# Kernel tuning notes

Measured on AMD Instinct MI355X. Metric: run time of the kernel, lower is better.

The kernel has to match this reference:

```python
import jax, jax.numpy as jnp
import numpy as np

L_DEG = 4      # max out-degree L
DEPTH = 7      # complete L-ary tree depth -> 21845 nodes
N_GEN = 16
C_ST = 8
M_LAB = 256


def _build_tree():
    sizes = [L_DEG ** d for d in range(DEPTH + 1)]
    limits = np.concatenate([[0], np.cumsum(sizes)]).astype(np.int64)
    t_size = int(limits[-1])
    nodes = np.arange(t_size)
    rng = np.random.default_rng(0)
    labels = rng.integers(0, M_LAB, t_size)
    parent = np.where(nodes > 0, (nodes - 1) // L_DEG, 0)
    pos = np.where(nodes > 0, (nodes - 1) % L_DEG, 0)
    ch = np.zeros((t_size, L_DEG), dtype=np.int64)
    n_internal = int(limits[-2])
    ch[:n_internal] = L_DEG * nodes[:n_internal, None] + np.arange(1, L_DEG + 1)[None, :]
    t = np.concatenate([labels[:, None], parent[:, None], pos[:, None], ch], axis=1).astype(np.int64)
    return t, limits


def setup_inputs() -> dict:
    key = jax.random.key(0)
    ka, kb, kp, ks = jax.random.split(key, 4)
    t, limits = _build_tree()
    return {
        "t": jnp.asarray(t),
        "t_limits": jnp.asarray(limits),
        "a": jax.random.normal(ka, (N_GEN, C_ST, C_ST, L_DEG), dtype=jnp.float32),
        "b": jax.random.normal(kb, (N_GEN, C_ST, M_LAB), dtype=jnp.float32),
        "pi": jax.random.normal(kp, (N_GEN, C_ST, L_DEG), dtype=jnp.float32),
        "sp": jax.random.normal(ks, (N_GEN, L_DEG), dtype=jnp.float32),
    }


def _forward(tn, lim, a, b, pi, sp):
    # tn, lim are host numpy int arrays (tree structure is a constant).
    G, C, _, L = a.shape
    t_size = int(lim[-1])
    n_levels = len(lim) - 1
    sL = int(lim[-2])                      # first leaf index
    labels = tn[:, 0]
    posf = tn[:, 2]
    ch_all = tn[:, 3:3 + L]

    sm_a = jax.nn.softmax(a, axis=1)       # P(parent_state i | child_state j, pos l)
    sm_b = jax.nn.softmax(b, axis=2)
    sm_pi = jax.nn.softmax(pi, axis=1)
    sm_sp = jax.nn.softmax(sp, axis=1)
    a_sp = sm_a * sm_sp[:, None, None, :]  # [G,i,j,L]

    # ---------------- upward pass ----------------
    prior = jnp.zeros((t_size, G, C), a.dtype)
    beta = jnp.zeros((t_size, G, C), a.dtype)
    beta_il = jnp.zeros((t_size, G, C), a.dtype)

    prior_lv = jnp.moveaxis(sm_pi[:, :, posf[sL:]], 2, 0)   # [NL,G,C]
    emis_lv = jnp.moveaxis(sm_b[:, :, labels[sL:]], 2, 0)   # [NL,G,C]
    beta_lv = prior_lv * emis_lv
    beta_lv = beta_lv / jnp.sum(beta_lv, axis=2, keepdims=True)
    prior = prior.at[sL:].set(prior_lv)
    beta = beta.at[sL:].set(beta_lv)

    for lev in range(n_levels - 2, -1, -1):   # internal levels, bottom-up
        s, e = int(lim[lev]), int(lim[lev + 1])
        ch = ch_all[s:e]                       # [P,L]
        mask = (ch > 0).astype(a.dtype)        # children packed in first slots
        prior_ch = prior[ch]                   # [P,L,G,C]
        beta_ch = beta[ch]                     # [P,L,G,C]
        u_prior = jnp.einsum('gijl,pl,plgj->pgi', a_sp, mask, prior_ch)
        u_bil = jnp.einsum('gijl,pl,plgj->pgi', a_sp, mask, beta_ch) / u_prior
        emis = jnp.moveaxis(sm_b[:, :, labels[s:e]], 2, 0)  # [P,G,C]
        tmp = emis * u_bil * u_prior
        u_beta = tmp / jnp.sum(tmp, axis=2, keepdims=True)
        prior = prior.at[s:e].set(u_prior)
        beta = beta.at[s:e].set(u_beta)
        beta_il = beta_il.at[s:e].set(u_bil)

    # ---------------- downward pass ----------------
    # row t_size is a dummy slot for padded (absent) children
    eps_i = jnp.zeros((t_size + 1, G, C), a.dtype).at[0].set(beta[0])
    eps_ijl = jnp.zeros((t_size, G, C, C, L), a.dtype)
    for lev in range(0, n_levels - 1):         # parents, top-down (root included)
        s, e = int(lim[lev]), int(lim[lev + 1])
        ch = ch_all[s:e]
        maskb = ch > 0
        mask = maskb.astype(a.dtype)
        beta_ch = jnp.transpose(beta[ch], (0, 2, 3, 1))       # [P,G,Cj,L]
        pe = eps_i[s:e] / (prior[s:e] * beta_il[s:e])         # [P,G,Ci]
        res = (pe[:, :, :, None, None] * a_sp[None]
               * beta_ch[:, :, None, :, :]
               * mask[:, None, None, None, :])                # [P,G,i,j,L]
        child_eps = jnp.sum(res, axis=3)                       # sum over j (as in source) -> [P,G,i,L]
        vals = jnp.moveaxis(child_eps, 3, 1).reshape(-1, G, C) # [P*L,G,C]
        safe = np.where(maskb, ch, t_size).reshape(-1)
        eps_i = eps_i.at[safe].set(vals)
        eps_ijl = eps_ijl.at[s:e].set(res)
    eps_i = eps_i[:t_size]
    # leaves' eps_ijl stay zero (source scatters zeros there)

    # ---------------- log-likelihood ----------------
    a_lh = jnp.einsum('ugijl,gijl->g', eps_ijl, jnp.log(sm_a))
    b_lh = jnp.einsum('ugc,gcu->g', eps_i, jnp.log(sm_b)[:, :, labels])
    pi_lh = jnp.einsum('ugc,gcu->g', eps_i[sL:], jnp.log(sm_pi)[:, :, posf[sL:]])
    eps_l = jnp.sum(eps_ijl, axis=(2, 3))                      # [u,g,L]
    sp_lh = jnp.einsum('ugl,gl->g', eps_l, jnp.log(sm_sp))
    return a_lh + b_lh + pi_lh + sp_lh


def reference(t, t_limits, a, b, pi, sp):
    tn = np.asarray(t)
    lim = np.asarray(t_limits)
    return _forward(tn, lim, a, b, pi, sp)
```

## Files before the change

### kernel.cpp

```cpp
#include <hip/hip_runtime.h>


#define G 16
#define C 8
#define GC 128
#define TSIZE 21845
#define SL 5461

__device__ __forceinline__ float grp8_sum(float v) {
  v += __shfl_xor(v, 1);
  v += __shfl_xor(v, 2);
  v += __shfl_xor(v, 4);
  return v;
}

__global__ void setup_kernel(const float* __restrict__ ain, const float* __restrict__ bin,
                             const float* __restrict__ piin, const float* __restrict__ spin,
                             float* __restrict__ a_sp, float* __restrict__ log_a,
                             float* __restrict__ sm_bT, float* __restrict__ log_bT,
                             float* __restrict__ sm_piT, float* __restrict__ log_piT,
                             float* __restrict__ log_sp, float* __restrict__ out) {
  int blk = blockIdx.x, tid = threadIdx.x;
  if (blk < 16) {
    int g = blk;
    __shared__ float red4[4];
    for (int c = 0; c < 8; ++c) {
      int row = g * 8 + c;
      float x = bin[row * 256 + tid];
      float m = x;
      #pragma unroll
      for (int off2 = 32; off2; off2 >>= 1) m = fmaxf(m, __shfl_xor(m, off2));
      if ((tid & 63) == 0) red4[tid >> 6] = m;
      __syncthreads();
      m = fmaxf(fmaxf(red4[0], red4[1]), fmaxf(red4[2], red4[3]));
      __syncthreads();
      float e = expf(x - m);
      float ssum = e;
      #pragma unroll
      for (int off2 = 32; off2; off2 >>= 1) ssum += __shfl_xor(ssum, off2);
      if ((tid & 63) == 0) red4[tid >> 6] = ssum;
      __syncthreads();
      ssum = red4[0] + red4[1] + red4[2] + red4[3];
      __syncthreads();
      sm_bT[tid * GC + row]  = e / ssum;
      log_bT[tid * GC + row] = (x - m) - logf(ssum);
    }
  } else if (blk == 16) {
    for (int col = tid; col < 512; col += 256) {
      int g = col >> 5, j = (col >> 2) & 7, l = col & 3;
      float x[8], m = -1e30f;
      #pragma unroll
      for (int i = 0; i < 8; ++i) { x[i] = ain[g*256 + i*32 + j*4 + l]; m = fmaxf(m, x[i]); }
      float ssum = 0.f;
      #pragma unroll
      for (int i = 0; i < 8; ++i) ssum += expf(x[i] - m);
      float ls = logf(ssum);
      float y0 = spin[g*4+0], y1 = spin[g*4+1], y2 = spin[g*4+2], y3 = spin[g*4+3];
      float ms = fmaxf(fmaxf(y0, y1), fmaxf(y2, y3));
      float d = expf(y0-ms) + expf(y1-ms) + expf(y2-ms) + expf(y3-ms);
      float spv = expf(spin[g*4+l] - ms) / d;
      #pragma unroll
      for (int i = 0; i < 8; ++i) {
        int o2 = g*256 + i*32 + j*4 + l;
        float smv = expf(x[i] - m) / ssum;
        a_sp[o2]  = smv * spv;
        log_a[o2] = (x[i] - m) - ls;
      }
    }
  } else {
    if (tid < 64) {
      int g = tid >> 2, l = tid & 3;
      float x[8], m = -1e30f;
      #pragma unroll
      for (int c = 0; c < 8; ++c) { x[c] = piin[g*32 + c*4 + l]; m = fmaxf(m, x[c]); }
      float ssum = 0.f;
      #pragma unroll
      for (int c = 0; c < 8; ++c) ssum += expf(x[c] - m);
      float ls = logf(ssum);
      #pragma unroll
      for (int c = 0; c < 8; ++c) {
        sm_piT[l*GC + g*8 + c]  = expf(x[c] - m) / ssum;
        log_piT[l*GC + g*8 + c] = (x[c] - m) - ls;
      }
    } else if (tid < 80) {
      int g = tid - 64;
      float y[4], m = -1e30f;
      #pragma unroll
      for (int l = 0; l < 4; ++l) { y[l] = spin[g*4 + l]; m = fmaxf(m, y[l]); }
      float ssum = 0.f;
      #pragma unroll
      for (int l = 0; l < 4; ++l) ssum += expf(y[l] - m);
      float ls = logf(ssum);
      #pragma unroll
      for (int l = 0; l < 4; ++l) log_sp[g*4 + l] = (y[l] - m) - ls;
    } else if (tid < 96) {
      out[tid - 80] = 0.0f;
    }
  }
}

__device__ __forceinline__ void up_lds(int v, int lab, int gi, int g8,
    const float* asp, const float* __restrict__ sm_bT,
    float* sBeta, float* sNum, bool wantNum) {
  int ch0 = 4*v + 1;
  float ub = 0.f;
  #pragma unroll
  for (int l = 0; l < 4; ++l) {
    const float4* bp = (const float4*)(sBeta + (ch0 + l)*GC + g8);
    float4 b0 = bp[0], b1 = bp[1];
    ub += asp[l]*b0.x + asp[4+l]*b0.y + asp[8+l]*b0.z + asp[12+l]*b0.w
        + asp[16+l]*b1.x + asp[20+l]*b1.y + asp[24+l]*b1.z + asp[28+l]*b1.w;
  }
  float tmp = sm_bT[lab*GC + gi] * ub;
  float s = grp8_sum(tmp);
  sBeta[v*GC + gi] = tmp / s;
  if (wantNum) sNum[v*GC + gi] = ub;
}

__device__ __forceinline__ double down_lds(int v, int lab, float e, int gi, int g8,
    const float* asp, const float* aal, const float* lsp,
    const float* __restrict__ log_bT, float* sBeta, const float* sNum) {
  float pe = e / sNum[v*GC + gi];
  int ch0 = 4*v + 1;
  float local = 0.f;
  #pragma unroll
  for (int l = 0; l < 4; ++l) {
    float4* bp = (float4*)(sBeta + (ch0 + l)*GC + g8);
    float4 b0 = bp[0], b1 = bp[1];
    float S = asp[l]*b0.x + asp[4+l]*b0.y + asp[8+l]*b0.z + asp[12+l]*b0.w
            + asp[16+l]*b1.x + asp[20+l]*b1.y + asp[24+l]*b1.z + asp[28+l]*b1.w;
    float A = aal[l]*b0.x + aal[4+l]*b0.y + aal[8+l]*b0.z + aal[12+l]*b0.w
            + aal[16+l]*b1.x + aal[20+l]*b1.y + aal[24+l]*b1.z + aal[28+l]*b1.w;
    float ce = pe * S;
    sBeta[(ch0 + l)*GC + gi] = ce;
    local += pe*A + ce*lsp[l];
  }
  return (double)local + (double)(e * log_bT[lab*GC + gi]);
}

__global__ __launch_bounds__(512, 1) void up_kernel(
    const float* __restrict__ a_sp, const float* __restrict__ sm_bT,
    const float* __restrict__ sm_piT, const int* __restrict__ t,
    float* __restrict__ betaG) {
  __shared__ float sBeta[85*GC];
  const int blk = blockIdx.x, tid = threadIdx.x;
  const int gi = tid & 127, g = gi >> 3, i = gi & 7, g8 = g*8, w = tid >> 7;
  float asp[32];
  {
    const float4* pa = (const float4*)(a_sp + g*256 + i*32);
    #pragma unroll
    for (int q = 0; q < 8; ++q) {
      float4 v = pa[q];
      asp[q*4+0]=v.x; asp[q*4+1]=v.y; asp[q*4+2]=v.z; asp[q*4+3]=v.w;
    }
  }
  const int base_leaf = SL + blk*64;
  #pragma unroll
  for (int it = 0; it < 16; ++it) {
    int k = it*4 + w;
    float bt = sm_piT[(k & 3)*GC + gi] * sm_bT[t[(base_leaf + k)*7]*GC + gi];
    float s = grp8_sum(bt);
    sBeta[(21 + k)*GC + gi] = bt / s;
  }
  __syncthreads();
  #pragma unroll
  for (int it = 0; it < 4; ++it) {
    int k = it*4 + w;
    up_lds(5 + k, t[(1365 + blk*16 + k)*7], gi, g8, asp, sm_bT, sBeta, nullptr, false);
  }
  __syncthreads();
  up_lds(1 + w, t[(341 + blk*4 + w)*7], gi, g8, asp, sm_bT, sBeta, nullptr, false);
  __syncthreads();
  if (tid < 128) {
    up_lds(0, t[(85 + blk)*7], gi, g8, asp, sm_bT, sBeta, nullptr, false);
    betaG[(size_t)(85 + blk)*GC + gi] = sBeta[gi];
  }
}

__global__ __launch_bounds__(512, 1) void downall_kernel(
    const float* __restrict__ a_sp, const float* __restrict__ log_a,
    const float* __restrict__ log_sp, const float* __restrict__ sm_bT,
    const float* __restrict__ log_bT, const float* __restrict__ sm_piT,
    const float* __restrict__ log_piT, const int* __restrict__ t,
    const float* __restrict__ betaG, float* __restrict__ out) {
  __shared__ float  sBeta[85*GC];
  __shared__ float  sNum[21*GC];
  __shared__ float  sEps[GC];
  __shared__ double sd[64];
  const int blk = blockIdx.x, tid = threadIdx.x;
  const int gi = tid & 127, g = gi >> 3, i = gi & 7, g8 = g*8, w = tid >> 7;
  float asp[32], aal[32], lsp[4];
  {
    const float4* pa = (const float4*)(a_sp  + g*256 + i*32);
    const float4* pl = (const float4*)(log_a + g*256 + i*32);
    #pragma unroll
    for (int k = 0; k < 8; ++k) {
      float4 va = pa[k], vl = pl[k];
      asp[k*4+0]=va.x; asp[k*4+1]=va.y; asp[k*4+2]=va.z; asp[k*4+3]=va.w;
      aal[k*4+0]=va.x*vl.x; aal[k*4+1]=va.y*vl.y; aal[k*4+2]=va.z*vl.z; aal[k*4+3]=va.w*vl.w;
    }
    #pragma unroll
    for (int l = 0; l < 4; ++l) lsp[l] = log_sp[g*4 + l];
  }

  #pragma unroll
  for (int it = 0; it < 16; ++it) {
    int k = it*4 + w, u = 21 + k;
    int ch0 = 4*u + 1;
    float ub = 0.f;
    #pragma unroll
    for (int l = 0; l < 4; ++l) {
      const float4* bp = (const float4*)(betaG + (size_t)(ch0 + l)*GC + g8);
      float4 b0 = bp[0], b1 = bp[1];
      ub += asp[l]*b0.x + asp[4+l]*b0.y + asp[8+l]*b0.z + asp[12+l]*b0.w
          + asp[16+l]*b1.x + asp[20+l]*b1.y + asp[24+l]*b1.z + asp[28+l]*b1.w;
    }
    float tmp = sm_bT[t[u*7]*GC + gi] * ub;
    float s = grp8_sum(tmp);
    sBeta[u*GC + gi] = tmp / s;
  }
  __syncthreads();
  #pragma unroll
  for (int it = 0; it < 4; ++it) {
    int u = 5 + it*4 + w;
    up_lds(u, t[u*7], gi, g8, asp, sm_bT, sBeta, sNum, true);
  }
  __syncthreads();
  up_lds(1 + w, t[(1 + w)*7], gi, g8, asp, sm_bT, sBeta, sNum, true);
  __syncthreads();
  if (tid < 128)
    up_lds(0, t[0], gi, g8, asp, sm_bT, sBeta, sNum, true);
  __syncthreads();

  if (tid < 128) {
    int a1 = 1 + (blk >> 6), a2 = 5 + (blk >> 4), a3 = 21 + (blk >> 2);
    float e = sBeta[gi];
    int anc[3] = {0, a1, a2};
    int chn[3] = {a1, a2, a3};
    #pragma unroll
    for (int s2 = 0; s2 < 3; ++s2) {
      float pe = e / sNum[anc[s2]*GC + gi];
      int l = (chn[s2] - 1) & 3;
      const float4* bp = (const float4*)(sBeta + chn[s2]*GC + g8);
      float4 b0 = bp[0], b1 = bp[1];
      float S = asp[l]*b0.x + asp[4+l]*b0.y + asp[8+l]*b0.z + asp[12+l]*b0.w
              + asp[16+l]*b1.x + asp[20+l]*b1.y + asp[24+l]*b1.z + asp[28+l]*b1.w;
      e = pe * S;
    }
    {
      float num3 = 0.f;
      int c30 = 4*a3 + 1;
      #pragma unroll
      for (int l = 0; l < 4; ++l) {
        const float4* bp = (const float4*)(betaG + (size_t)(c30 + l)*GC + g8);
        float4 b0 = bp[0], b1 = bp[1];
        num3 += asp[l]*b0.x + asp[4+l]*b0.y + asp[8+l]*b0.z + asp[12+l]*b0.w
              + asp[16+l]*b1.x + asp[20+l]*b1.y + asp[24+l]*b1.z + asp[28+l]*b1.w;
      }
      float pe = e / num3;
      int l = blk & 3;
      const float4* bp = (const float4*)(betaG + (size_t)(85 + blk)*GC + g8);
      float4 b0 = bp[0], b1 = bp[1];
      float S = asp[l]*b0.x + asp[4+l]*b0.y + asp[8+l]*b0.z + asp[12+l]*b0.w
              + asp[16+l]*b1.x + asp[20+l]*b1.y + asp[24+l]*b1.z + asp[28+l]*b1.w;
      e = pe * S;
    }
    sEps[gi] = e;
  }
  __syncthreads();

  if (blk == 0) {
    double acc0 = 0.0;
    if (tid < 128)
      acc0 += down_lds(0, t[0], sBeta[gi], gi, g8, asp, aal, lsp, log_bT, sBeta, sNum);
    __syncthreads();
    {
      int v = 1 + w;
      acc0 += down_lds(v, t[v*7], sBeta[v*GC + gi], gi, g8, asp, aal, lsp, log_bT, sBeta, sNum);
    }
    __syncthreads();
    #pragma unroll
    for (int it = 0; it < 4; ++it) {
      int v = 5 + it*4 + w;
      acc0 += down_lds(v, t[v*7], sBeta[v*GC + gi], gi, g8, asp, aal, lsp, log_bT, sBeta, sNum);
    }
    __syncthreads();
    #pragma unroll
    for (int it = 0; it < 16; ++it) {
      int k = it*4 + w, u = 21 + k;
      float e = sBeta[u*GC + gi];
      int ch0 = 4*u + 1;
      float Sv[4], Av[4], num = 0.f;
      #pragma unroll
      for (int l = 0; l < 4; ++l) {
        const float4* bp = (const float4*)(betaG + (size_t)(ch0 + l)*GC + g8);
        float4 b0 = bp[0], b1 = bp[1];
        Sv[l] = asp[l]*b0.x + asp[4+l]*b0.y + asp[8+l]*b0.z + asp[12+l]*b0.w
              + asp[16+l]*b1.x + asp[20+l]*b1.y + asp[24+l]*b1.z + asp[28+l]*b1.w;
        Av[l] = aal[l]*b0.x + aal[4+l]*b0.y + aal[8+l]*b0.z + aal[12+l]*b0.w
              + aal[16+l]*b1.x + aal[20+l]*b1.y + aal[24+l]*b1.z + aal[28+l]*b1.w;
        num += Sv[l];
      }
      float pe = e / num;
      float local = 0.f;
      #pragma unroll
      for (int l = 0; l < 4; ++l) {
        float ce = pe * Sv[l];
        local += pe*Av[l] + ce*lsp[l];
      }
      acc0 += (double)local + (double)(e * log_bT[t[u*7]*GC + gi]);
    }
    acc0 += __shfl_xor(acc0, 1);
    acc0 += __shfl_xor(acc0, 2);
    acc0 += __shfl_xor(acc0, 4);
    if (i == 0) sd[tid >> 3] = acc0;
    __syncthreads();
    if (tid < 16) {
      double s = sd[tid] + sd[16 + tid] + sd[32 + tid] + sd[48 + tid];
      atomicAdd(&out[tid], (float)s);
    }
    __syncthreads();
  }

  const int base_leaf = SL + blk*64;
  #pragma unroll
  for (int it = 0; it < 16; ++it) {
    int k = it*4 + w;
    float bt = sm_piT[(k & 3)*GC + gi] * sm_bT[t[(base_leaf + k)*7]*GC + gi];
    float s = grp8_sum(bt);
    sBeta[(21 + k)*GC + gi] = bt / s;
  }
  __syncthreads();
  #pragma unroll
  for (int it = 0; it < 4; ++it) {
    int k = it*4 + w;
    up_lds(5 + k, t[(1365 + blk*16 + k)*7], gi, g8, asp, sm_bT, sBeta, sNum, true);
  }
  __syncthreads();
  up_lds(1 + w, t[(341 + blk*4 + w)*7], gi, g8, asp, sm_bT, sBeta, sNum, true);
  __syncthreads();

  double acc = 0.0;
  if (tid < 128) {
    up_lds(0, t[(85 + blk)*7], gi, g8, asp, sm_bT, sBeta, sNum, true);
    acc += down_lds(0, t[(85 + blk)*7], sEps[gi], gi, g8, asp, aal, lsp,
                    log_bT, sBeta, sNum);
  }
  __syncthreads();
  {
    int v = 1 + w;
    acc += down_lds(v, t[(341 + blk*4 + w)*7], sBeta[v*GC + gi], gi, g8,
                    asp, aal, lsp, log_bT, sBeta, sNum);
  }
  __syncthreads();
  #pragma unroll
  for (int it = 0; it < 4; ++it) {
    int k = it*4 + w, v = 5 + k;
    acc += down_lds(v, t[(1365 + blk*16 + k)*7], sBeta[v*GC + gi], gi, g8,
                    asp, aal, lsp, log_bT, sBeta, sNum);
  }
  __syncthreads();
  #pragma unroll
  for (int it = 0; it < 16; ++it) {
    int k = it*4 + w;
    float e = sBeta[(21 + k)*GC + gi];
    acc += (double)(e * (log_bT[t[(base_leaf + k)*7]*GC + gi] +
                         log_piT[(k & 3)*GC + gi]));
  }
  acc += __shfl_xor(acc, 1);
  acc += __shfl_xor(acc, 2);
  acc += __shfl_xor(acc, 4);
  if (i == 0) sd[tid >> 3] = acc;
  __syncthreads();
  if (tid < 16) {
    double s = sd[tid] + sd[16 + tid] + sd[32 + tid] + sd[48 + tid];
    atomicAdd(&out[tid], (float)s);
  }
}

extern "C" void kernel_launch(void* const* d_in, const int* in_sizes, int n_in,
                              void* d_out, int out_size, void* d_ws, size_t ws_size,
                              hipStream_t stream) {
  const int*   t  = (const int*)d_in[0];
  const float* a  = (const float*)d_in[2];
  const float* b  = (const float*)d_in[3];
  const float* pi = (const float*)d_in[4];
  const float* sp = (const float*)d_in[5];
  float* out = (float*)d_out;

  char* w = (char*)d_ws;
  size_t off = 0;
  auto carve = [&](size_t bytes) -> void* {
    void* ptr = w + off;
    off += (bytes + 255) & ~(size_t)255;
    return ptr;
  };
  float* a_sp    = (float*)carve((size_t)16*8*8*4*4);
  float* log_a   = (float*)carve((size_t)16*8*8*4*4);
  float* sm_bT   = (float*)carve((size_t)256*GC*4);
  float* log_bT  = (float*)carve((size_t)256*GC*4);
  float* sm_piT  = (float*)carve((size_t)4*GC*4);
  float* log_piT = (float*)carve((size_t)4*GC*4);
  float* log_sp  = (float*)carve((size_t)16*4*4);
  float* betaG   = (float*)carve((size_t)341*GC*4);

  setup_kernel<<<18, 256, 0, stream>>>(a, b, pi, sp, a_sp, log_a, sm_bT, log_bT,
                                       sm_piT, log_piT, log_sp, out);
  up_kernel<<<256, 512, 0, stream>>>(a_sp, sm_bT, sm_piT, t, betaG);
  downall_kernel<<<256, 512, 0, stream>>>(a_sp, log_a, log_sp, sm_bT, log_bT,
                                          sm_piT, log_piT, t, betaG, out);
}
```

Baseline: 115.6 us.

## Fuse setup, up and down passes into one cooperative kernel with grid syncs

Replaces the three kernel launches with a single cooperative kernel that uses grid-wide syncs between the setup, upward-subtree and top/downward phases. Each block keeps its subtree beta and normalizer arrays in LDS across the grid sync, so the down phase no longer recomputes the subtree upward pass. The float atomicAdd output is replaced by per-block double partials reduced deterministically by block 0 after a final grid sync. The setup work is also spread over more blocks. The cost is three grid barriers, plus higher LDS use per block that must still allow all 256 blocks to be co-resident.

Result: slower. 330.5 us (+185.9%).

```diff
diff --git a/kernel.cpp b/kernel.cpp
--- a/kernel.cpp
+++ b/kernel.cpp
@@ -1,10 +1,12 @@
 #include <hip/hip_runtime.h>
+#include <hip/hip_cooperative_groups.h>
+
+namespace cg = cooperative_groups;
 
 
 #define G 16
 #define C 8
 #define GC 128
-#define TSIZE 21845
 #define SL 5461
 
 __device__ __forceinline__ float grp8_sum(float v) {
@@ -12,91 +14,6 @@
   v += __shfl_xor(v, 2);
   v += __shfl_xor(v, 4);
   return v;
-}
-
-__global__ void setup_kernel(const float* __restrict__ ain, const float* __restrict__ bin,
-                             const float* __restrict__ piin, const float* __restrict__ spin,
-                             float* __restrict__ a_sp, float* __restrict__ log_a,
-                             float* __restrict__ sm_bT, float* __restrict__ log_bT,
-                             float* __restrict__ sm_piT, float* __restrict__ log_piT,
-                             float* __restrict__ log_sp, float* __restrict__ out) {
-  int blk = blockIdx.x, tid = threadIdx.x;
-  if (blk < 16) {
-    int g = blk;
-    __shared__ float red4[4];
-    for (int c = 0; c < 8; ++c) {
-      int row = g * 8 + c;
-      float x = bin[row * 256 + tid];
-      float m = x;
-      #pragma unroll
-      for (int off2 = 32; off2; off2 >>= 1) m = fmaxf(m, __shfl_xor(m, off2));
-      if ((tid & 63) == 0) red4[tid >> 6] = m;
-      __syncthreads();
-      m = fmaxf(fmaxf(red4[0], red4[1]), fmaxf(red4[2], red4[3]));
-      __syncthreads();
-      float e = expf(x - m);
-      float ssum = e;
-      #pragma unroll
-      for (int off2 = 32; off2; off2 >>= 1) ssum += __shfl_xor(ssum, off2);
-      if ((tid & 63) == 0) red4[tid >> 6] = ssum;
-      __syncthreads();
-      ssum = red4[0] + red4[1] + red4[2] + red4[3];
-      __syncthreads();
-      sm_bT[tid * GC + row]  = e / ssum;
-      log_bT[tid * GC + row] = (x - m) - logf(ssum);
-    }
-  } else if (blk == 16) {
-    for (int col = tid; col < 512; col += 256) {
-      int g = col >> 5, j = (col >> 2) & 7, l = col & 3;
-      float x[8], m = -1e30f;
-      #pragma unroll
-      for (int i = 0; i < 8; ++i) { x[i] = ain[g*256 + i*32 + j*4 + l]; m = fmaxf(m, x[i]); }
-      float ssum = 0.f;
-      #pragma unroll
-      for (int i = 0; i < 8; ++i) ssum += expf(x[i] - m);
-      float ls = logf(ssum);
-      float y0 = spin[g*4+0], y1 = spin[g*4+1], y2 = spin[g*4+2], y3 = spin[g*4+3];
-      float ms = fmaxf(fmaxf(y0, y1), fmaxf(y2, y3));
-      float d = expf(y0-ms) + expf(y1-ms) + expf(y2-ms) + expf(y3-ms);
-      float spv = expf(spin[g*4+l] - ms) / d;
-      #pragma unroll
-      for (int i = 0; i < 8; ++i) {
-        int o2 = g*256 + i*32 + j*4 + l;
-        float smv = expf(x[i] - m) / ssum;
-        a_sp[o2]  = smv * spv;
-        log_a[o2] = (x[i] - m) - ls;
-      }
-    }
-  } else {
-    if (tid < 64) {
-      int g = tid >> 2, l = tid & 3;
-      float x[8], m = -1e30f;
-      #pragma unroll
-      for (int c = 0; c < 8; ++c) { x[c] = piin[g*32 + c*4 + l]; m = fmaxf(m, x[c]); }
-      float ssum = 0.f;
-      #pragma unroll
-      for (int c = 0; c < 8; ++c) ssum += expf(x[c] - m);
-      float ls = logf(ssum);
-      #pragma unroll
-      for (int c = 0; c < 8; ++c) {
-        sm_piT[l*GC + g*8 + c]  = expf(x[c] - m) / ssum;
-        log_piT[l*GC + g*8 + c] = (x[c] - m) - ls;
-      }
-    } else if (tid < 80) {
-      int g = tid - 64;
-      float y[4], m = -1e30f;
-      #pragma unroll
-      for (int l = 0; l < 4; ++l) { y[l] = spin[g*4 + l]; m = fmaxf(m, y[l]); }
-      float ssum = 0.f;
-      #pragma unroll
-      for (int l = 0; l < 4; ++l) ssum += expf(y[l] - m);
-      float ls = logf(ssum);
-      #pragma unroll
-      for (int l = 0; l < 4; ++l) log_sp[g*4 + l] = (y[l] - m) - ls;
-    } else if (tid < 96) {
-      out[tid - 80] = 0.0f;
-    }
-  }
 }
 
 __device__ __forceinline__ void up_lds(int v, int lab, int gi, int g8,
@@ -138,70 +55,139 @@
   return (double)local + (double)(e * log_bT[lab*GC + gi]);
 }
 
-__global__ __launch_bounds__(512, 1) void up_kernel(
-    const float* __restrict__ a_sp, const float* __restrict__ sm_bT,
-    const float* __restrict__ sm_piT, const int* __restrict__ t,
-    float* __restrict__ betaG) {
-  __shared__ float sBeta[85*GC];
+__global__ __launch_bounds__(512, 1) void fused_kernel(
+    const int* __restrict__ t,
+    const float* __restrict__ ain, const float* __restrict__ bin,
+    const float* __restrict__ piin, const float* __restrict__ spin,
+    float* __restrict__ a_sp, float* __restrict__ log_a,
+    float* __restrict__ sm_bT, float* __restrict__ log_bT,
+    float* __restrict__ sm_piT, float* __restrict__ log_piT,
+    float* __restrict__ log_sp, float* __restrict__ betaG,
+    double* __restrict__ partial, float* __restrict__ out) {
+  cg::grid_group grid = cg::this_grid();
+
+  __shared__ float  sBetaSub[85*GC];
+  __shared__ float  sNumSub[21*GC];
+  __shared__ float  sBetaTop[85*GC];
+  __shared__ float  sNumTop[21*GC];
+  __shared__ double sd[64];
+  __shared__ double sfin[256];
+  __shared__ float  red8[8];
+
   const int blk = blockIdx.x, tid = threadIdx.x;
   const int gi = tid & 127, g = gi >> 3, i = gi & 7, g8 = g*8, w = tid >> 7;
-  float asp[32];
+
+  if (blk < 128) {
+    int row = blk;
+    int lab = tid & 255;
+    float x = bin[row*256 + lab];
+    float m = x;
+    #pragma unroll
+    for (int off = 32; off; off >>= 1) m = fmaxf(m, __shfl_xor(m, off));
+    if ((tid & 63) == 0) red8[tid >> 6] = m;
+    __syncthreads();
+    m = fmaxf(fmaxf(red8[0], red8[1]), fmaxf(red8[2], red8[3]));
+    __syncthreads();
+    float e = expf(x - m);
+    float ssum = e;
+    #pragma unroll
+    for (int off = 32; off; off >>= 1) ssum += __shfl_xor(ssum, off);
+    if ((tid & 63) == 0) red8[tid >> 6] = ssum;
+    __syncthreads();
+    ssum = red8[0] + red8[1] + red8[2] + red8[3];
+    if (tid < 256) {
+      sm_bT[lab*GC + row]  = e / ssum;
+      log_bT[lab*GC + row] = (x - m) - logf(ssum);
+    }
+  } else if (blk == 128) {
+    int col = tid;
+    int gg = col >> 5, jj = (col >> 2) & 7, ll = col & 3;
+    float x[8], m = -1e30f;
+    #pragma unroll
+    for (int ii = 0; ii < 8; ++ii) { x[ii] = ain[gg*256 + ii*32 + jj*4 + ll]; m = fmaxf(m, x[ii]); }
+    float ssum = 0.f;
+    #pragma unroll
+    for (int ii = 0; ii < 8; ++ii) ssum += expf(x[ii] - m);
+    float ls = logf(ssum);
+    float y0 = spin[gg*4+0], y1 = spin[gg*4+1], y2 = spin[gg*4+2], y3 = spin[gg*4+3];
+    float ms = fmaxf(fmaxf(y0, y1), fmaxf(y2, y3));
+    float d = expf(y0-ms) + expf(y1-ms) + expf(y2-ms) + expf(y3-ms);
+    float spv = expf(spin[gg*4+ll] - ms) / d;
+    #pragma unroll
+    for (int ii = 0; ii < 8; ++ii) {
+      int o2 = gg*256 + ii*32 + jj*4 + ll;
+      float smv = expf(x[ii] - m) / ssum;
+      a_sp[o2]  = smv * spv;
+      log_a[o2] = (x[ii] - m) - ls;
+    }
+  } else if (blk == 129) {
+    if (tid < 64) {
+      int gg = tid >> 2, ll = tid & 3;
+      float x[8], m = -1e30f;
+      #pragma unroll
+      for (int c = 0; c < 8; ++c) { x[c] = piin[gg*32 + c*4 + ll]; m = fmaxf(m, x[c]); }
+      float ssum = 0.f;
+      #pragma unroll
+      for (int c = 0; c < 8; ++c) ssum += expf(x[c] - m);
+      float ls = logf(ssum);
+      #pragma unroll
+      for (int c = 0; c < 8; ++c) {
+        sm_piT[ll*GC + gg*8 + c]  = expf(x[c] - m) / ssum;
+        log_piT[ll*GC + gg*8 + c] = (x[c] - m) - ls;
+      }
+    } else if (tid < 80) {
+      int gg = tid - 64;
+      float y[4], m = -1e30f;
+      #pragma unroll
+      for (int l = 0; l < 4; ++l) { y[l] = spin[gg*4 + l]; m = fmaxf(m, y[l]); }
+      float ssum = 0.f;
+      #pragma unroll
+      for (int l = 0; l < 4; ++l) ssum += expf(y[l] - m);
+      float ls = logf(ssum);
+      #pragma unroll
+      for (int l = 0; l < 4; ++l) log_sp[gg*4 + l] = (y[l] - m) - ls;
+    }
+  }
+  __threadfence();
+  grid.sync();
+
+  float asp[32], aal[32], lsp[4];
   {
-    const float4* pa = (const float4*)(a_sp + g*256 + i*32);
-    #pragma unroll
-    for (int q = 0; q < 8; ++q) {
-      float4 v = pa[q];
-      asp[q*4+0]=v.x; asp[q*4+1]=v.y; asp[q*4+2]=v.z; asp[q*4+3]=v.w;
-    }
-  }
+    const float4* pa = (const float4*)(a_sp  + g*256 + i*32);
+    const float4* pl = (const float4*)(log_a + g*256 + i*32);
+    #pragma unroll
+    for (int k = 0; k < 8; ++k) {
+      float4 va = pa[k], vl = pl[k];
+      asp[k*4+0]=va.x; asp[k*4+1]=va.y; asp[k*4+2]=va.z; asp[k*4+3]=va.w;
+      aal[k*4+0]=va.x*vl.x; aal[k*4+1]=va.y*vl.y; aal[k*4+2]=va.z*vl.z; aal[k*4+3]=va.w*vl.w;
+    }
+    #pragma unroll
+    for (int l = 0; l < 4; ++l) lsp[l] = log_sp[g*4 + l];
+  }
+
   const int base_leaf = SL + blk*64;
   #pragma unroll
   for (int it = 0; it < 16; ++it) {
     int k = it*4 + w;
     float bt = sm_piT[(k & 3)*GC + gi] * sm_bT[t[(base_leaf + k)*7]*GC + gi];
     float s = grp8_sum(bt);
-    sBeta[(21 + k)*GC + gi] = bt / s;
+    sBetaSub[(21 + k)*GC + gi] = bt / s;
   }
   __syncthreads();
   #pragma unroll
   for (int it = 0; it < 4; ++it) {
     int k = it*4 + w;
-    up_lds(5 + k, t[(1365 + blk*16 + k)*7], gi, g8, asp, sm_bT, sBeta, nullptr, false);
-  }
-  __syncthreads();
-  up_lds(1 + w, t[(341 + blk*4 + w)*7], gi, g8, asp, sm_bT, sBeta, nullptr, false);
+    up_lds(5 + k, t[(1365 + blk*16 + k)*7], gi, g8, asp, sm_bT, sBetaSub, sNumSub, true);
+  }
+  __syncthreads();
+  up_lds(1 + w, t[(341 + blk*4 + w)*7], gi, g8, asp, sm_bT, sBetaSub, sNumSub, true);
   __syncthreads();
   if (tid < 128) {
-    up_lds(0, t[(85 + blk)*7], gi, g8, asp, sm_bT, sBeta, nullptr, false);
-    betaG[(size_t)(85 + blk)*GC + gi] = sBeta[gi];
-  }
-}
-
-__global__ __launch_bounds__(512, 1) void downall_kernel(
-    const float* __restrict__ a_sp, const float* __restrict__ log_a,
-    const float* __restrict__ log_sp, const float* __restrict__ sm_bT,
-    const float* __restrict__ log_bT, const float* __restrict__ sm_piT,
-    const float* __restrict__ log_piT, const int* __restrict__ t,
-    const float* __restrict__ betaG, float* __restrict__ out) {
-  __shared__ float  sBeta[85*GC];
-  __shared__ float  sNum[21*GC];
-  __shared__ float  sEps[GC];
-  __shared__ double sd[64];
-  const int blk = blockIdx.x, tid = threadIdx.x;
-  const int gi = tid & 127, g = gi >> 3, i = gi & 7, g8 = g*8, w = tid >> 7;
-  float asp[32], aal[32], lsp[4];
-  {
-    const float4* pa = (const float4*)(a_sp  + g*256 + i*32);
-    const float4* pl = (const float4*)(log_a + g*256 + i*32);
-    #pragma unroll
-    for (int k = 0; k < 8; ++k) {
-      float4 va = pa[k], vl = pl[k];
-      asp[k*4+0]=va.x; asp[k*4+1]=va.y; asp[k*4+2]=va.z; asp[k*4+3]=va.w;
-      aal[k*4+0]=va.x*vl.x; aal[k*4+1]=va.y*vl.y; aal[k*4+2]=va.z*vl.z; aal[k*4+3]=va.w*vl.w;
-    }
-    #pragma unroll
-    for (int l = 0; l < 4; ++l) lsp[l] = log_sp[g*4 + l];
-  }
+    up_lds(0, t[(85 + blk)*7], gi, g8, asp, sm_bT, sBetaSub, sNumSub, true);
+    betaG[(size_t)(85 + blk)*GC + gi] = sBetaSub[gi];
+  }
+  __threadfence();
+  grid.sync();
 
   #pragma unroll
   for (int it = 0; it < 16; ++it) {
@@ -217,164 +203,126 @@
     }
     float tmp = sm_bT[t[u*7]*GC + gi] * ub;
     float s = grp8_sum(tmp);
-    sBeta[u*GC + gi] = tmp / s;
+    sBetaTop[u*GC + gi] = tmp / s;
   }
   __syncthreads();
   #pragma unroll
   for (int it = 0; it < 4; ++it) {
     int u = 5 + it*4 + w;
-    up_lds(u, t[u*7], gi, g8, asp, sm_bT, sBeta, sNum, true);
-  }
-  __syncthreads();
-  up_lds(1 + w, t[(1 + w)*7], gi, g8, asp, sm_bT, sBeta, sNum, true);
+    up_lds(u, t[u*7], gi, g8, asp, sm_bT, sBetaTop, sNumTop, true);
+  }
+  __syncthreads();
+  up_lds(1 + w, t[(1 + w)*7], gi, g8, asp, sm_bT, sBetaTop, sNumTop, true);
   __syncthreads();
   if (tid < 128)
-    up_lds(0, t[0], gi, g8, asp, sm_bT, sBeta, sNum, true);
-  __syncthreads();
-
+    up_lds(0, t[0], gi, g8, asp, sm_bT, sBetaTop, sNumTop, true);
+  __syncthreads();
+
+  double acc = 0.0;
+  float eRoot = 0.f;
   if (tid < 128) {
     int a1 = 1 + (blk >> 6), a2 = 5 + (blk >> 4), a3 = 21 + (blk >> 2);
-    float e = sBeta[gi];
+    float e = sBetaTop[gi];
     int anc[3] = {0, a1, a2};
     int chn[3] = {a1, a2, a3};
     #pragma unroll
     for (int s2 = 0; s2 < 3; ++s2) {
-      float pe = e / sNum[anc[s2]*GC + gi];
+      float pe = e / sNumTop[anc[s2]*GC + gi];
       int l = (chn[s2] - 1) & 3;
-      const float4* bp = (const float4*)(sBeta + chn[s2]*GC + g8);
+      const float4* bp = (const float4*)(sBetaTop + chn[s2]*GC + g8);
       float4 b0 = bp[0], b1 = bp[1];
       float S = asp[l]*b0.x + asp[4+l]*b0.y + asp[8+l]*b0.z + asp[12+l]*b0.w
               + asp[16+l]*b1.x + asp[20+l]*b1.y + asp[24+l]*b1.z + asp[28+l]*b1.w;
       e = pe * S;
     }
-    {
-      float num3 = 0.f;
-      int c30 = 4*a3 + 1;
-      #pragma unroll
-      for (int l = 0; l < 4; ++l) {
-        const float4* bp = (const float4*)(betaG + (size_t)(c30 + l)*GC + g8);
-        float4 b0 = bp[0], b1 = bp[1];
-        num3 += asp[l]*b0.x + asp[4+l]*b0.y + asp[8+l]*b0.z + asp[12+l]*b0.w
-              + asp[16+l]*b1.x + asp[20+l]*b1.y + asp[24+l]*b1.z + asp[28+l]*b1.w;
-      }
-      float pe = e / num3;
-      int l = blk & 3;
-      const float4* bp = (const float4*)(betaG + (size_t)(85 + blk)*GC + g8);
+    float Sv[4], Av[4], num3 = 0.f;
+    int c30 = 4*a3 + 1;
+    #pragma unroll
+    for (int l = 0; l < 4; ++l) {
+      const float4* bp = (const float4*)(betaG + (size_t)(c30 + l)*GC + g8);
       float4 b0 = bp[0], b1 = bp[1];
-      float S = asp[l]*b0.x + asp[4+l]*b0.y + asp[8+l]*b0.z + asp[12+l]*b0.w
-              + asp[16+l]*b1.x + asp[20+l]*b1.y + asp[24+l]*b1.z + asp[28+l]*b1.w;
-      e = pe * S;
-    }
-    sEps[gi] = e;
-  }
-  __syncthreads();
+      Sv[l] = asp[l]*b0.x + asp[4+l]*b0.y + asp[8+l]*b0.z + asp[12+l]*b0.w
+            + asp[16+l]*b1.x + asp[20+l]*b1.y + asp[24+l]*b1.z + asp[28+l]*b1.w;
+      num3 += Sv[l];
+      Av[l] = aal[l]*b0.x + aal[4+l]*b0.y + aal[8+l]*b0.z + aal[12+l]*b0.w
+            + aal[16+l]*b1.x + aal[20+l]*b1.y + aal[24+l]*b1.z + aal[28+l]*b1.w;
+    }
+    float e3 = e;
+    float pe3 = e3 / num3;
+    eRoot = pe3 * Sv[blk & 3];
+    if ((blk & 3) == 0) {
+      float local = 0.f;
+      #pragma unroll
+      for (int l = 0; l < 4; ++l) local += pe3*Av[l] + (pe3*Sv[l])*lsp[l];
+      acc += (double)local + (double)(e3 * log_bT[t[a3*7]*GC + gi]);
+    }
+  }
 
   if (blk == 0) {
-    double acc0 = 0.0;
     if (tid < 128)
-      acc0 += down_lds(0, t[0], sBeta[gi], gi, g8, asp, aal, lsp, log_bT, sBeta, sNum);
+      acc += down_lds(0, t[0], sBetaTop[gi], gi, g8, asp, aal, lsp, log_bT, sBetaTop, sNumTop);
     __syncthreads();
     {
       int v = 1 + w;
-      acc0 += down_lds(v, t[v*7], sBeta[v*GC + gi], gi, g8, asp, aal, lsp, log_bT, sBeta, sNum);
+      acc += down_lds(v, t[v*7], sBetaTop[v*GC + gi], gi, g8, asp, aal, lsp, log_bT, sBetaTop, sNumTop);
     }
     __syncthreads();
     #pragma unroll
     for (int it = 0; it < 4; ++it) {
       int v = 5 + it*4 + w;
-      acc0 += down_lds(v, t[v*7], sBeta[v*GC + gi], gi, g8, asp, aal, lsp, log_bT, sBeta, sNum);
-    }
-    __syncthreads();
-    #pragma unroll
-    for (int it = 0; it < 16; ++it) {
-      int k = it*4 + w, u = 21 + k;
-      float e = sBeta[u*GC + gi];
-      int ch0 = 4*u + 1;
-      float Sv[4], Av[4], num = 0.f;
-      #pragma unroll
-      for (int l = 0; l < 4; ++l) {
-        const float4* bp = (const float4*)(betaG + (size_t)(ch0 + l)*GC + g8);
-        float4 b0 = bp[0], b1 = bp[1];
-        Sv[l] = asp[l]*b0.x + asp[4+l]*b0.y + asp[8+l]*b0.z + asp[12+l]*b0.w
-              + asp[16+l]*b1.x + asp[20+l]*b1.y + asp[24+l]*b1.z + asp[28+l]*b1.w;
-        Av[l] = aal[l]*b0.x + aal[4+l]*b0.y + aal[8+l]*b0.z + aal[12+l]*b0.w
-              + aal[16+l]*b1.x + aal[20+l]*b1.y + aal[24+l]*b1.z + aal[28+l]*b1.w;
-        num += Sv[l];
-      }
-      float pe = e / num;
-      float local = 0.f;
-      #pragma unroll
-      for (int l = 0; l < 4; ++l) {
-        float ce = pe * Sv[l];
-        local += pe*Av[l] + ce*lsp[l];
-      }
-      acc0 += (double)local + (double)(e * log_bT[t[u*7]*GC + gi]);
-    }
-    acc0 += __shfl_xor(acc0, 1);
-    acc0 += __shfl_xor(acc0, 2);
-    acc0 += __shfl_xor(acc0, 4);
-    if (i == 0) sd[tid >> 3] = acc0;
-    __syncthreads();
-    if (tid < 16) {
-      double s = sd[tid] + sd[16 + tid] + sd[32 + tid] + sd[48 + tid];
-      atomicAdd(&out[tid], (float)s);
-    }
-    __syncthreads();
-  }
-
-  const int base_leaf = SL + blk*64;
+      acc += down_lds(v, t[v*7], sBetaTop[v*GC + gi], gi, g8, asp, aal, lsp, log_bT, sBetaTop, sNumTop);
+    }
+  }
+
+  if (tid < 128)
+    acc += down_lds(0, t[(85 + blk)*7], eRoot, gi, g8, asp, aal, lsp, log_bT, sBetaSub, sNumSub);
+  __syncthreads();
+  {
+    int v = 1 + w;
+    acc += down_lds(v, t[(341 + blk*4 + w)*7], sBetaSub[v*GC + gi], gi, g8,
+                    asp, aal, lsp, log_bT, sBetaSub, sNumSub);
+  }
+  __syncthreads();
+  #pragma unroll
+  for (int it = 0; it < 4; ++it) {
+    int k = it*4 + w, v = 5 + k;
+    acc += down_lds(v, t[(1365 + blk*16 + k)*7], sBetaSub[v*GC + gi], gi, g8,
+                    asp, aal, lsp, log_bT, sBetaSub, sNumSub);
+  }
+  __syncthreads();
   #pragma unroll
   for (int it = 0; it < 16; ++it) {
     int k = it*4 + w;
-    float bt = sm_piT[(k & 3)*GC + gi] * sm_bT[t[(base_leaf + k)*7]*GC + gi];
-    float s = grp8_sum(bt);
-    sBeta[(21 + k)*GC + gi] = bt / s;
-  }
-  __syncthreads();
-  #pragma unroll
-  for (int it = 0; it < 4; ++it) {
-    int k = it*4 + w;
-    up_lds(5 + k, t[(1365 + blk*16 + k)*7], gi, g8, asp, sm_bT, sBeta, sNum, true);
-  }
-  __syncthreads();
-  up_lds(1 + w, t[(341 + blk*4 + w)*7], gi, g8, asp, sm_bT, sBeta, sNum, true);
-  __syncthreads();
-
-  double acc = 0.0;
-  if (tid < 128) {
-    up_lds(0, t[(85 + blk)*7], gi, g8, asp, sm_bT, sBeta, sNum, true);
-    acc += down_lds(0, t[(85 + blk)*7], sEps[gi], gi, g8, asp, aal, lsp,
-                    log_bT, sBeta, sNum);
-  }
-  __syncthreads();
-  {
-    int v = 1 + w;
-    acc += down_lds(v, t[(341 + blk*4 + w)*7], sBeta[v*GC + gi], gi, g8,
-                    asp, aal, lsp, log_bT, sBeta, sNum);
-  }
-  __syncthreads();
-  #pragma unroll
-  for (int it = 0; it < 4; ++it) {
-    int k = it*4 + w, v = 5 + k;
-    acc += down_lds(v, t[(1365 + blk*16 + k)*7], sBeta[v*GC + gi], gi, g8,
-                    asp, aal, lsp, log_bT, sBeta, sNum);
-  }
-  __syncthreads();
-  #pragma unroll
-  for (int it = 0; it < 16; ++it) {
-    int k = it*4 + w;
-    float e = sBeta[(21 + k)*GC + gi];
+    float e = sBetaSub[(21 + k)*GC + gi];
     acc += (double)(e * (log_bT[t[(base_leaf + k)*7]*GC + gi] +
                          log_piT[(k & 3)*GC + gi]));
   }
+
   acc += __shfl_xor(acc, 1);
   acc += __shfl_xor(acc, 2);
   acc += __shfl_xor(acc, 4);
   if (i == 0) sd[tid >> 3] = acc;
   __syncthreads();
-  if (tid < 16) {
-    double s = sd[tid] + sd[16 + tid] + sd[32 + tid] + sd[48 + tid];
-    atomicAdd(&out[tid], (float)s);
+  if (tid < 16) partial[blk*16 + tid] = sd[tid] + sd[16 + tid] + sd[32 + tid] + sd[48 + tid];
+  __threadfence();
+  grid.sync();
+
+  if (blk == 0) {
+    if (tid < 256) {
+      int gg = tid & 15, ch = tid >> 4;
+      const double* p = partial + (size_t)ch*256 + gg;
+      double s = 0.0;
+      #pragma unroll
+      for (int q = 0; q < 16; ++q) s += p[q*16];
+      sfin[tid] = s;
+    }
+    __syncthreads();
+    if (tid < 16) {
+      double tot = 0.0;
+      #pragma unroll
+      for (int ch = 0; ch < 16; ++ch) tot += sfin[ch*16 + tid];
+      out[tid] = (float)tot;
+    }
   }
 }
 
@@ -388,25 +336,27 @@
   const float* sp = (const float*)d_in[5];
   float* out = (float*)d_out;
 
-  char* w = (char*)d_ws;
+  char* wsp = (char*)d_ws;
   size_t off = 0;
   auto carve = [&](size_t bytes) -> void* {
-    void* ptr = w + off;
+    void* ptr = wsp + off;
     off += (bytes + 255) & ~(size_t)255;
     return ptr;
   };
-  float* a_sp    = (float*)carve((size_t)16*8*8*4*4);
-  float* log_a   = (float*)carve((size_t)16*8*8*4*4);
-  float* sm_bT   = (float*)carve((size_t)256*GC*4);
-  float* log_bT  = (float*)carve((size_t)256*GC*4);
-  float* sm_piT  = (float*)carve((size_t)4*GC*4);
-  float* log_piT = (float*)carve((size_t)4*GC*4);
-  float* log_sp  = (float*)carve((size_t)16*4*4);
-  float* betaG   = (float*)carve((size_t)341*GC*4);
-
-  setup_kernel<<<18, 256, 0, stream>>>(a, b, pi, sp, a_sp, log_a, sm_bT, log_bT,
-                                       sm_piT, log_piT, log_sp, out);
-  up_kernel<<<256, 512, 0, stream>>>(a_sp, sm_bT, sm_piT, t, betaG);
-  downall_kernel<<<256, 512, 0, stream>>>(a_sp, log_a, log_sp, sm_bT, log_bT,
-                                          sm_piT, log_piT, t, betaG, out);
-}
+  float*  a_sp    = (float*)carve((size_t)16*8*8*4*4);
+  float*  log_a   = (float*)carve((size_t)16*8*8*4*4);
+  float*  sm_bT   = (float*)carve((size_t)256*GC*4);
+  float*  log_bT  = (float*)carve((size_t)256*GC*4);
+  float*  sm_piT  = (float*)carve((size_t)4*GC*4);
+  float*  log_piT = (float*)carve((size_t)4*GC*4);
+  float*  log_sp  = (float*)carve((size_t)16*4*4);
+  float*  betaG   = (float*)carve((size_t)341*GC*4);
+  double* partial = (double*)carve((size_t)256*16*8);
+
+  void* kargs[] = { (void*)&t, (void*)&a, (void*)&b, (void*)&pi, (void*)&sp,
+                    (void*)&a_sp, (void*)&log_a, (void*)&sm_bT, (void*)&log_bT,
+                    (void*)&sm_piT, (void*)&log_piT, (void*)&log_sp,
+                    (void*)&betaG, (void*)&partial, (void*)&out };
+  hipLaunchCooperativeKernel((const void*)fused_kernel, dim3(256), dim3(512),
+                             kargs, 0, stream);
+}
```

## Spread level-3 node eps work across blocks and use last-block reduction

Applied to the files above, without the earlier changes.

The level-3 (nodes 21..84) log-likelihood terms were computed serially by block 0 in a 16-iteration loop. They are now computed by each owning block (the one with blk&3==0), which removes the serial tail on block 0. Cross-block accumulation switches from per-block float atomics to double partials, with a final reduction done by the last block to arrive, detected through an agent-scope atomic counter. This adds a counter and a partials buffer and gives a deterministic double-precision final sum.

Result: faster. 111.0 us (-3.9%).

```diff
diff --git a/kernel.cpp b/kernel.cpp
--- a/kernel.cpp
+++ b/kernel.cpp
@@ -19,7 +19,7 @@
                              float* __restrict__ a_sp, float* __restrict__ log_a,
                              float* __restrict__ sm_bT, float* __restrict__ log_bT,
                              float* __restrict__ sm_piT, float* __restrict__ log_piT,
-                             float* __restrict__ log_sp, float* __restrict__ out) {
+                             float* __restrict__ log_sp, unsigned* __restrict__ ctr) {
   int blk = blockIdx.x, tid = threadIdx.x;
   if (blk < 16) {
     int g = blk;
@@ -93,8 +93,8 @@
       float ls = logf(ssum);
       #pragma unroll
       for (int l = 0; l < 4; ++l) log_sp[g*4 + l] = (y[l] - m) - ls;
-    } else if (tid < 96) {
-      out[tid - 80] = 0.0f;
+    } else if (tid == 80) {
+      *ctr = 0u;
     }
   }
 }
@@ -182,11 +182,14 @@
     const float* __restrict__ log_sp, const float* __restrict__ sm_bT,
     const float* __restrict__ log_bT, const float* __restrict__ sm_piT,
     const float* __restrict__ log_piT, const int* __restrict__ t,
-    const float* __restrict__ betaG, float* __restrict__ out) {
+    const float* __restrict__ betaG, unsigned* __restrict__ ctr,
+    double* __restrict__ partial, float* __restrict__ out) {
   __shared__ float  sBeta[85*GC];
   __shared__ float  sNum[21*GC];
   __shared__ float  sEps[GC];
   __shared__ double sd[64];
+  __shared__ double sfin[256];
+  __shared__ unsigned lastFlag;
   const int blk = blockIdx.x, tid = threadIdx.x;
   const int gi = tid & 127, g = gi >> 3, i = gi & 7, g8 = g*8, w = tid >> 7;
   float asp[32], aal[32], lsp[4];
@@ -232,6 +235,7 @@
     up_lds(0, t[0], gi, g8, asp, sm_bT, sBeta, sNum, true);
   __syncthreads();
 
+  double acc = 0.0;
   if (tid < 128) {
     int a1 = 1 + (blk >> 6), a2 = 5 + (blk >> 4), a3 = 21 + (blk >> 2);
     float e = sBeta[gi];
@@ -247,77 +251,43 @@
               + asp[16+l]*b1.x + asp[20+l]*b1.y + asp[24+l]*b1.z + asp[28+l]*b1.w;
       e = pe * S;
     }
-    {
-      float num3 = 0.f;
-      int c30 = 4*a3 + 1;
-      #pragma unroll
-      for (int l = 0; l < 4; ++l) {
-        const float4* bp = (const float4*)(betaG + (size_t)(c30 + l)*GC + g8);
-        float4 b0 = bp[0], b1 = bp[1];
-        num3 += asp[l]*b0.x + asp[4+l]*b0.y + asp[8+l]*b0.z + asp[12+l]*b0.w
-              + asp[16+l]*b1.x + asp[20+l]*b1.y + asp[24+l]*b1.z + asp[28+l]*b1.w;
-      }
-      float pe = e / num3;
-      int l = blk & 3;
-      const float4* bp = (const float4*)(betaG + (size_t)(85 + blk)*GC + g8);
+    float Sv[4], Av[4], num3 = 0.f;
+    int c30 = 4*a3 + 1;
+    #pragma unroll
+    for (int l = 0; l < 4; ++l) {
+      const float4* bp = (const float4*)(betaG + (size_t)(c30 + l)*GC + g8);
       float4 b0 = bp[0], b1 = bp[1];
-      float S = asp[l]*b0.x + asp[4+l]*b0.y + asp[8+l]*b0.z + asp[12+l]*b0.w
-              + asp[16+l]*b1.x + asp[20+l]*b1.y + asp[24+l]*b1.z + asp[28+l]*b1.w;
-      e = pe * S;
-    }
-    sEps[gi] = e;
+      Sv[l] = asp[l]*b0.x + asp[4+l]*b0.y + asp[8+l]*b0.z + asp[12+l]*b0.w
+            + asp[16+l]*b1.x + asp[20+l]*b1.y + asp[24+l]*b1.z + asp[28+l]*b1.w;
+      num3 += Sv[l];
+      Av[l] = aal[l]*b0.x + aal[4+l]*b0.y + aal[8+l]*b0.z + aal[12+l]*b0.w
+            + aal[16+l]*b1.x + aal[20+l]*b1.y + aal[24+l]*b1.z + aal[28+l]*b1.w;
+    }
+    float e3 = e;
+    float pe3 = e3 / num3;
+    sEps[gi] = pe3 * Sv[blk & 3];
+    if ((blk & 3) == 0) {
+      float local = 0.f;
+      #pragma unroll
+      for (int l = 0; l < 4; ++l) local += pe3*Av[l] + (pe3*Sv[l])*lsp[l];
+      acc += (double)local + (double)(e3 * log_bT[t[a3*7]*GC + gi]);
+    }
   }
   __syncthreads();
 
   if (blk == 0) {
-    double acc0 = 0.0;
     if (tid < 128)
-      acc0 += down_lds(0, t[0], sBeta[gi], gi, g8, asp, aal, lsp, log_bT, sBeta, sNum);
+      acc += down_lds(0, t[0], sBeta[gi], gi, g8, asp, aal, lsp, log_bT, sBeta, sNum);
     __syncthreads();
     {
       int v = 1 + w;
-      acc0 += down_lds(v, t[v*7], sBeta[v*GC + gi], gi, g8, asp, aal, lsp, log_bT, sBeta, sNum);
+      acc += down_lds(v, t[v*7], sBeta[v*GC + gi], gi, g8, asp, aal, lsp, log_bT, sBeta, sNum);
     }
     __syncthreads();
     #pragma unroll
     for (int it = 0; it < 4; ++it) {
       int v = 5 + it*4 + w;
-      acc0 += down_lds(v, t[v*7], sBeta[v*GC + gi], gi, g8, asp, aal, lsp, log_bT, sBeta, sNum);
-    }
-    __syncthreads();
-    #pragma unroll
-    for (int it = 0; it < 16; ++it) {
-      int k = it*4 + w, u = 21 + k;
-      float e = sBeta[u*GC + gi];
-      int ch0 = 4*u + 1;
-      float Sv[4], Av[4], num = 0.f;
-      #pragma unroll
-      for (int l = 0; l < 4; ++l) {
-        const float4* bp = (const float4*)(betaG + (size_t)(ch0 + l)*GC + g8);
-        float4 b0 = bp[0], b1 = bp[1];
-        Sv[l] = asp[l]*b0.x + asp[4+l]*b0.y + asp[8+l]*b0.z + asp[12+l]*b0.w
-              + asp[16+l]*b1.x + asp[20+l]*b1.y + asp[24+l]*b1.z + asp[28+l]*b1.w;
-        Av[l] = aal[l]*b0.x + aal[4+l]*b0.y + aal[8+l]*b0.z + aal[12+l]*b0.w
-              + aal[16+l]*b1.x + aal[20+l]*b1.y + aal[24+l]*b1.z + aal[28+l]*b1.w;
-        num += Sv[l];
-      }
-      float pe = e / num;
-      float local = 0.f;
-      #pragma unroll
-      for (int l = 0; l < 4; ++l) {
-        float ce = pe * Sv[l];
-        local += pe*Av[l] + ce*lsp[l];
-      }
-      acc0 += (double)local + (double)(e * log_bT[t[u*7]*GC + gi]);
-    }
-    acc0 += __shfl_xor(acc0, 1);
-    acc0 += __shfl_xor(acc0, 2);
-    acc0 += __shfl_xor(acc0, 4);
-    if (i == 0) sd[tid >> 3] = acc0;
-    __syncthreads();
-    if (tid < 16) {
-      double s = sd[tid] + sd[16 + tid] + sd[32 + tid] + sd[48 + tid];
-      atomicAdd(&out[tid], (float)s);
+      acc += down_lds(v, t[v*7], sBeta[v*GC + gi], gi, g8, asp, aal, lsp, log_bT, sBeta, sNum);
     }
     __syncthreads();
   }
@@ -340,7 +310,6 @@
   up_lds(1 + w, t[(341 + blk*4 + w)*7], gi, g8, asp, sm_bT, sBeta, sNum, true);
   __syncthreads();
 
-  double acc = 0.0;
   if (tid < 128) {
     up_lds(0, t[(85 + blk)*7], gi, g8, asp, sm_bT, sBeta, sNum, true);
     acc += down_lds(0, t[(85 + blk)*7], sEps[gi], gi, g8, asp, aal, lsp,
@@ -367,14 +336,37 @@
     acc += (double)(e * (log_bT[t[(base_leaf + k)*7]*GC + gi] +
                          log_piT[(k & 3)*GC + gi]));
   }
+
   acc += __shfl_xor(acc, 1);
   acc += __shfl_xor(acc, 2);
   acc += __shfl_xor(acc, 4);
   if (i == 0) sd[tid >> 3] = acc;
   __syncthreads();
-  if (tid < 16) {
-    double s = sd[tid] + sd[16 + tid] + sd[32 + tid] + sd[48 + tid];
-    atomicAdd(&out[tid], (float)s);
+  if (tid < 16) partial[blk*16 + tid] = sd[tid] + sd[16 + tid] + sd[32 + tid] + sd[48 + tid];
+  __syncthreads();
+
+  if (tid == 0) {
+    unsigned old = __hip_atomic_fetch_add(ctr, 1u, __ATOMIC_ACQ_REL,
+                                          __HIP_MEMORY_SCOPE_AGENT);
+    lastFlag = (old == 255u);
+  }
+  __syncthreads();
+  if (lastFlag) {
+    if (tid < 256) {
+      int gg = tid & 15, ch = tid >> 4;
+      const double* p = partial + (size_t)ch*256 + gg;
+      double s = 0.0;
+      #pragma unroll
+      for (int q = 0; q < 16; ++q) s += p[q*16];
+      sfin[tid] = s;
+    }
+    __syncthreads();
+    if (tid < 16) {
+      double tot = 0.0;
+      #pragma unroll
+      for (int ch = 0; ch < 16; ++ch) tot += sfin[ch*16 + tid];
+      out[tid] = (float)tot;
+    }
   }
 }
 
@@ -395,18 +387,21 @@
     off += (bytes + 255) & ~(size_t)255;
     return ptr;
   };
-  float* a_sp    = (float*)carve((size_t)16*8*8*4*4);
-  float* log_a   = (float*)carve((size_t)16*8*8*4*4);
-  float* sm_bT   = (float*)carve((size_t)256*GC*4);
-  float* log_bT  = (float*)carve((size_t)256*GC*4);
-  float* sm_piT  = (float*)carve((size_t)4*GC*4);
-  float* log_piT = (float*)carve((size_t)4*GC*4);
-  float* log_sp  = (float*)carve((size_t)16*4*4);
-  float* betaG   = (float*)carve((size_t)341*GC*4);
+  float*    a_sp    = (float*)carve((size_t)16*8*8*4*4);
+  float*    log_a   = (float*)carve((size_t)16*8*8*4*4);
+  float*    sm_bT   = (float*)carve((size_t)256*GC*4);
+  float*    log_bT  = (float*)carve((size_t)256*GC*4);
+  float*    sm_piT  = (float*)carve((size_t)4*GC*4);
+  float*    log_piT = (float*)carve((size_t)4*GC*4);
+  float*    log_sp  = (float*)carve((size_t)16*4*4);
+  float*    betaG   = (float*)carve((size_t)341*GC*4);
+  double*   partial = (double*)carve((size_t)256*16*8);
+  unsigned* ctr     = (unsigned*)carve((size_t)4);
 
   setup_kernel<<<18, 256, 0, stream>>>(a, b, pi, sp, a_sp, log_a, sm_bT, log_bT,
-                                       sm_piT, log_piT, log_sp, out);
+                                       sm_piT, log_piT, log_sp, ctr);
   up_kernel<<<256, 512, 0, stream>>>(a_sp, sm_bT, sm_piT, t, betaG);
   downall_kernel<<<256, 512, 0, stream>>>(a_sp, log_a, log_sp, sm_bT, log_bT,
-                                          sm_piT, log_piT, t, betaG, out);
-}
+                                          sm_piT, log_piT, t, betaG, ctr,
+                                          partial, out);
+}
```
